# Kernel tuning notes

Measured on AMD Instinct MI355X. Metric: run time of the kernel, lower is better.

The kernel has to match this reference:

```python
import jax, jax.numpy as jnp
import numpy as np

N = 8192  # number of DAG nodes


def setup_inputs() -> dict:
    key = jax.random.key(0)
    k1, k2, k3 = jax.random.split(key, 3)
    thresholds = jax.random.normal(k1, (N,), dtype=jnp.float32)
    # children in [-1, N): -1 marks a leaf (no child)
    left = jax.random.randint(k2, (N,), -1, N, dtype=jnp.int32)
    right = jax.random.randint(k3, (N,), -1, N, dtype=jnp.int32)
    return {"thresholds": thresholds, "left": left, "right": right}


def reference(thresholds, left, right):
    # BFS fixed-point reachability from node 0, N sequential relaxation steps.
    n_nodes = left.shape[0]

    def step(reachable, _):
        # route children of reachable non-leaf nodes into a scatter; dump
        # inactive slots into the sentinel index n_nodes (dropped on slice)
        active_left = jnp.where(reachable & (left >= 0), left, n_nodes)
        active_right = jnp.where(reachable & (right >= 0), right, n_nodes)
        new_reachable = jnp.zeros(n_nodes + 1, dtype=jnp.bool_)
        new_reachable = new_reachable.at[active_left].set(True)
        new_reachable = new_reachable.at[active_right].set(True)
        new_reachable = new_reachable.at[0].set(True)
        return (new_reachable[:n_nodes] | reachable, None)

    init = jnp.zeros(n_nodes, dtype=jnp.bool_).at[0].set(True)
    mask, _ = jax.lax.scan(step, init, None, length=n_nodes)
    return mask
```

## Files before the change

kernel.cpp:

```cpp
#include <hip/hip_runtime.h>


#define NMAX   8192
#define BLK    256
#define NWORDS (NMAX / 32)
#define INNER  4

__global__ __launch_bounds__(BLK) void dag_reach_kernel(
    const int* __restrict__ left,
    const int* __restrict__ right,
    int* __restrict__ out,
    int n)
{
    __shared__ int2 sLR[NMAX];
    __shared__ unsigned int reach[NWORDS];
    __shared__ int s_changed;

    const int tid = threadIdx.x;

    for (int i = 4 * tid; i < n; i += 4 * BLK) {
        int4 l4 = *reinterpret_cast<const int4*>(left  + i);
        int4 r4 = *reinterpret_cast<const int4*>(right + i);
        sLR[i + 0] = make_int2(l4.x, r4.x);
        sLR[i + 1] = make_int2(l4.y, r4.y);
        sLR[i + 2] = make_int2(l4.z, r4.z);
        sLR[i + 3] = make_int2(l4.w, r4.w);
    }
    reach[tid] = (tid == 0) ? 1u : 0u;
    __syncthreads();

    unsigned int expanded = 0u;
    const int base = tid * 32;
    volatile unsigned int* vreach = reach;

    while (true) {
        if (tid == 0) s_changed = 0;
        __syncthreads();

        int localChanged = 0;
        #pragma unroll
        for (int it = 0; it < INNER; ++it) {
            unsigned int pend = vreach[tid] & ~expanded;
            if (pend) {
                localChanged = 1;
                expanded |= pend;
                while (pend) {
                    int b0 = __ffs(pend) - 1; pend &= pend - 1;
                    int b1 = -1, b2 = -1, b3 = -1;
                    if (pend) { b1 = __ffs(pend) - 1; pend &= pend - 1;
                        if (pend) { b2 = __ffs(pend) - 1; pend &= pend - 1;
                            if (pend) { b3 = __ffs(pend) - 1; pend &= pend - 1; } } }
                    int2 lr0 = sLR[base + b0];
                    int2 lr1 = sLR[base + (b1 < 0 ? b0 : b1)];
                    int2 lr2 = sLR[base + (b2 < 0 ? b0 : b2)];
                    int2 lr3 = sLR[base + (b3 < 0 ? b0 : b3)];
                    if (lr0.x >= 0) atomicOr(&reach[lr0.x >> 5], 1u << (lr0.x & 31));
                    if (lr0.y >= 0) atomicOr(&reach[lr0.y >> 5], 1u << (lr0.y & 31));
                    if (b1 >= 0) {
                        if (lr1.x >= 0) atomicOr(&reach[lr1.x >> 5], 1u << (lr1.x & 31));
                        if (lr1.y >= 0) atomicOr(&reach[lr1.y >> 5], 1u << (lr1.y & 31));
                    }
                    if (b2 >= 0) {
                        if (lr2.x >= 0) atomicOr(&reach[lr2.x >> 5], 1u << (lr2.x & 31));
                        if (lr2.y >= 0) atomicOr(&reach[lr2.y >> 5], 1u << (lr2.y & 31));
                    }
                    if (b3 >= 0) {
                        if (lr3.x >= 0) atomicOr(&reach[lr3.x >> 5], 1u << (lr3.x & 31));
                        if (lr3.y >= 0) atomicOr(&reach[lr3.y >> 5], 1u << (lr3.y & 31));
                    }
                }
            }
        }
        if (localChanged) s_changed = 1;
        __syncthreads();
        if (!s_changed) break;
    }

    for (int i = 4 * tid; i < n; i += 4 * BLK) {
        const unsigned w = reach[i >> 5];
        const int b = i & 31;
        *reinterpret_cast<int4*>(out + i) =
            make_int4((int)((w >> (b + 0)) & 1u),
                      (int)((w >> (b + 1)) & 1u),
                      (int)((w >> (b + 2)) & 1u),
                      (int)((w >> (b + 3)) & 1u));
    }
}

extern "C" void kernel_launch(void* const* d_in, const int* in_sizes, int n_in,
                              void* d_out, int out_size, void* d_ws, size_t ws_size,
                              hipStream_t stream)
{
    const int* left  = (const int*)d_in[1];
    const int* right = (const int*)d_in[2];
    int* out = (int*)d_out;
    const int n = in_sizes[1];

    dag_reach_kernel<<<1, BLK, 0, stream>>>(left, right, out, n);
}
```

Baseline: 74.89 us.

## Run BFS expansion in a single wavefront to drop block-wide barriers

The frontier expansion now runs on one 64-lane wavefront, with each lane owning 128 nodes (four bitmap words). Termination is decided by a wavefront vote (__any) instead of a shared flag plus two __syncthreads per round. This removes block barrier and flag overhead from the long sequential propagation chain. In exchange only 64 lanes do the work and each lane walks up to four times as many pending bits, which lowers parallelism per round.

After: 96.17 us. 1.28x slower.

```diff
diff --git a/kernel.cpp b/kernel.cpp
--- a/kernel.cpp
+++ b/kernel.cpp
@@ -4,7 +4,6 @@
 #define NMAX   8192
 #define BLK    256
 #define NWORDS (NMAX / 32)
-#define INNER  4
 
 __global__ __launch_bounds__(BLK) void dag_reach_kernel(
     const int* __restrict__ left,
@@ -14,7 +13,6 @@
 {
     __shared__ int2 sLR[NMAX];
     __shared__ unsigned int reach[NWORDS];
-    __shared__ int s_changed;
 
     const int tid = threadIdx.x;
 
@@ -26,55 +24,60 @@
         sLR[i + 2] = make_int2(l4.z, r4.z);
         sLR[i + 3] = make_int2(l4.w, r4.w);
     }
-    reach[tid] = (tid == 0) ? 1u : 0u;
+    for (int i = tid; i < NWORDS; i += BLK) reach[i] = (i == 0) ? 1u : 0u;
     __syncthreads();
 
-    unsigned int expanded = 0u;
-    const int base = tid * 32;
-    volatile unsigned int* vreach = reach;
+    if (tid < 64) {
+        const int lane  = tid;
+        const int wbase = lane * 4;
+        const int nbase = lane * 128;
+        unsigned int exp0 = 0u, exp1 = 0u, exp2 = 0u, exp3 = 0u;
+        volatile unsigned int* vreach = reach;
 
-    while (true) {
-        if (tid == 0) s_changed = 0;
-        __syncthreads();
+        while (true) {
+            unsigned int p0 = vreach[wbase + 0] & ~exp0;
+            unsigned int p1 = vreach[wbase + 1] & ~exp1;
+            unsigned int p2 = vreach[wbase + 2] & ~exp2;
+            unsigned int p3 = vreach[wbase + 3] & ~exp3;
+            unsigned long long pa = ((unsigned long long)p1 << 32) | p0;
+            unsigned long long pb = ((unsigned long long)p3 << 32) | p2;
+            if (!__any((pa | pb) != 0ull)) break;
+            exp0 |= p0; exp1 |= p1; exp2 |= p2; exp3 |= p3;
 
-        int localChanged = 0;
-        #pragma unroll
-        for (int it = 0; it < INNER; ++it) {
-            unsigned int pend = vreach[tid] & ~expanded;
-            if (pend) {
-                localChanged = 1;
-                expanded |= pend;
-                while (pend) {
-                    int b0 = __ffs(pend) - 1; pend &= pend - 1;
+            #pragma unroll
+            for (int half = 0; half < 2; ++half) {
+                unsigned long long p = half ? pb : pa;
+                const int nb = nbase + (half << 6);
+                while (p) {
+                    int b0 = __ffsll(p) - 1; p &= p - 1;
                     int b1 = -1, b2 = -1, b3 = -1;
-                    if (pend) { b1 = __ffs(pend) - 1; pend &= pend - 1;
-                        if (pend) { b2 = __ffs(pend) - 1; pend &= pend - 1;
-                            if (pend) { b3 = __ffs(pend) - 1; pend &= pend - 1; } } }
-                    int2 lr0 = sLR[base + b0];
-                    int2 lr1 = sLR[base + (b1 < 0 ? b0 : b1)];
-                    int2 lr2 = sLR[base + (b2 < 0 ? b0 : b2)];
-                    int2 lr3 = sLR[base + (b3 < 0 ? b0 : b3)];
-                    if (lr0.x >= 0) atomicOr(&reach[lr0.x >> 5], 1u << (lr0.x & 31));
-                    if (lr0.y >= 0) atomicOr(&reach[lr0.y >> 5], 1u << (lr0.y & 31));
+                    if (p) { b1 = __ffsll(p) - 1; p &= p - 1;
+                        if (p) { b2 = __ffsll(p) - 1; p &= p - 1;
+                            if (p) { b3 = __ffsll(p) - 1; p &= p - 1; } } }
+                    int2 e0 = sLR[nb + b0];
+                    int2 e1 = sLR[nb + (b1 < 0 ? b0 : b1)];
+                    int2 e2 = sLR[nb + (b2 < 0 ? b0 : b2)];
+                    int2 e3 = sLR[nb + (b3 < 0 ? b0 : b3)];
+                    if (e0.x >= 0) atomicOr(&reach[e0.x >> 5], 1u << (e0.x & 31));
+                    if (e0.y >= 0) atomicOr(&reach[e0.y >> 5], 1u << (e0.y & 31));
                     if (b1 >= 0) {
-                        if (lr1.x >= 0) atomicOr(&reach[lr1.x >> 5], 1u << (lr1.x & 31));
-                        if (lr1.y >= 0) atomicOr(&reach[lr1.y >> 5], 1u << (lr1.y & 31));
+                        if (e1.x >= 0) atomicOr(&reach[e1.x >> 5], 1u << (e1.x & 31));
+                        if (e1.y >= 0) atomicOr(&reach[e1.y >> 5], 1u << (e1.y & 31));
                     }
                     if (b2 >= 0) {
-                        if (lr2.x >= 0) atomicOr(&reach[lr2.x >> 5], 1u << (lr2.x & 31));
-                        if (lr2.y >= 0) atomicOr(&reach[lr2.y >> 5], 1u << (lr2.y & 31));
+                        if (e2.x >= 0) atomicOr(&reach[e2.x >> 5], 1u << (e2.x & 31));
+                        if (e2.y >= 0) atomicOr(&reach[e2.y >> 5], 1u << (e2.y & 31));
                     }
                     if (b3 >= 0) {
-                        if (lr3.x >= 0) atomicOr(&reach[lr3.x >> 5], 1u << (lr3.x & 31));
-                        if (lr3.y >= 0) atomicOr(&reach[lr3.y >> 5], 1u << (lr3.y & 31));
+                        if (e3.x >= 0) atomicOr(&reach[e3.x >> 5], 1u << (e3.x & 31));
+                        if (e3.y >= 0) atomicOr(&reach[e3.y >> 5], 1u << (e3.y & 31));
                     }
                 }
             }
+            __threadfence_block();
         }
-        if (localChanged) s_changed = 1;
-        __syncthreads();
-        if (!s_changed) break;
     }
+    __syncthreads();
 
     for (int i = 4 * tid; i < n; i += 4 * BLK) {
         const unsigned w = reach[i >> 5];
```

## Use 1024 threads with 8 nodes each and a triple-buffered convergence flag

Applied to the files above, without the earlier changes.

Raises the block size from 256 to 1024 threads, so each thread owns 8 nodes (a byte of a reach word) instead of 32. This shortens the per-thread serial expansion loop on the critical path. The change flag is now rotated across three shared slots and written once per wavefront via __any, which removes one __syncthreads per outer iteration. The cost is more threads contending on the shared atomics and a heavier barrier with 16 waves instead of 4.

After: 74.33 us. About the same (-0.8%).

```diff
diff --git a/kernel.cpp b/kernel.cpp
--- a/kernel.cpp
+++ b/kernel.cpp
@@ -2,7 +2,7 @@
 
 
 #define NMAX   8192
-#define BLK    256
+#define BLK    1024
 #define NWORDS (NMAX / 32)
 #define INNER  4
 
@@ -14,35 +14,49 @@
 {
     __shared__ int2 sLR[NMAX];
     __shared__ unsigned int reach[NWORDS];
-    __shared__ int s_changed;
+    __shared__ int s_flag[3];
 
     const int tid = threadIdx.x;
 
-    for (int i = 4 * tid; i < n; i += 4 * BLK) {
-        int4 l4 = *reinterpret_cast<const int4*>(left  + i);
-        int4 r4 = *reinterpret_cast<const int4*>(right + i);
-        sLR[i + 0] = make_int2(l4.x, r4.x);
-        sLR[i + 1] = make_int2(l4.y, r4.y);
-        sLR[i + 2] = make_int2(l4.z, r4.z);
-        sLR[i + 3] = make_int2(l4.w, r4.w);
+    {
+        const int i = 8 * tid;
+        if (i + 7 < n) {
+            int4 l0 = *reinterpret_cast<const int4*>(left  + i);
+            int4 l1 = *reinterpret_cast<const int4*>(left  + i + 4);
+            int4 r0 = *reinterpret_cast<const int4*>(right + i);
+            int4 r1 = *reinterpret_cast<const int4*>(right + i + 4);
+            sLR[i + 0] = make_int2(l0.x, r0.x);
+            sLR[i + 1] = make_int2(l0.y, r0.y);
+            sLR[i + 2] = make_int2(l0.z, r0.z);
+            sLR[i + 3] = make_int2(l0.w, r0.w);
+            sLR[i + 4] = make_int2(l1.x, r1.x);
+            sLR[i + 5] = make_int2(l1.y, r1.y);
+            sLR[i + 6] = make_int2(l1.z, r1.z);
+            sLR[i + 7] = make_int2(l1.w, r1.w);
+        } else {
+            for (int k = i; k < n; ++k) sLR[k] = make_int2(left[k], right[k]);
+        }
     }
-    reach[tid] = (tid == 0) ? 1u : 0u;
+    if (tid < NWORDS) reach[tid] = (tid == 0) ? 1u : 0u;
+    if (tid < 3)      s_flag[tid] = 0;
     __syncthreads();
 
+    const int word_idx = tid >> 2;
+    const int shift    = (tid & 3) * 8;
+    const int base     = tid * 8;
     unsigned int expanded = 0u;
-    const int base = tid * 32;
     volatile unsigned int* vreach = reach;
 
+    int p3 = 0;
     while (true) {
-        if (tid == 0) s_changed = 0;
-        __syncthreads();
+        const int pn3 = (p3 == 2) ? 0 : p3 + 1;
+        int ch = 0;
 
-        int localChanged = 0;
         #pragma unroll
         for (int it = 0; it < INNER; ++it) {
-            unsigned int pend = vreach[tid] & ~expanded;
+            unsigned int pend = ((vreach[word_idx] >> shift) & 0xFFu) & ~expanded;
             if (pend) {
-                localChanged = 1;
+                ch = 1;
                 expanded |= pend;
                 while (pend) {
                     int b0 = __ffs(pend) - 1; pend &= pend - 1;
@@ -50,30 +64,33 @@
                     if (pend) { b1 = __ffs(pend) - 1; pend &= pend - 1;
                         if (pend) { b2 = __ffs(pend) - 1; pend &= pend - 1;
                             if (pend) { b3 = __ffs(pend) - 1; pend &= pend - 1; } } }
-                    int2 lr0 = sLR[base + b0];
-                    int2 lr1 = sLR[base + (b1 < 0 ? b0 : b1)];
-                    int2 lr2 = sLR[base + (b2 < 0 ? b0 : b2)];
-                    int2 lr3 = sLR[base + (b3 < 0 ? b0 : b3)];
-                    if (lr0.x >= 0) atomicOr(&reach[lr0.x >> 5], 1u << (lr0.x & 31));
-                    if (lr0.y >= 0) atomicOr(&reach[lr0.y >> 5], 1u << (lr0.y & 31));
+                    int2 e0 = sLR[base + b0];
+                    int2 e1 = sLR[base + (b1 < 0 ? b0 : b1)];
+                    int2 e2 = sLR[base + (b2 < 0 ? b0 : b2)];
+                    int2 e3 = sLR[base + (b3 < 0 ? b0 : b3)];
+                    if (e0.x >= 0) atomicOr(&reach[e0.x >> 5], 1u << (e0.x & 31));
+                    if (e0.y >= 0) atomicOr(&reach[e0.y >> 5], 1u << (e0.y & 31));
                     if (b1 >= 0) {
-                        if (lr1.x >= 0) atomicOr(&reach[lr1.x >> 5], 1u << (lr1.x & 31));
-                        if (lr1.y >= 0) atomicOr(&reach[lr1.y >> 5], 1u << (lr1.y & 31));
+                        if (e1.x >= 0) atomicOr(&reach[e1.x >> 5], 1u << (e1.x & 31));
+                        if (e1.y >= 0) atomicOr(&reach[e1.y >> 5], 1u << (e1.y & 31));
                     }
                     if (b2 >= 0) {
-                        if (lr2.x >= 0) atomicOr(&reach[lr2.x >> 5], 1u << (lr2.x & 31));
-                        if (lr2.y >= 0) atomicOr(&reach[lr2.y >> 5], 1u << (lr2.y & 31));
+                        if (e2.x >= 0) atomicOr(&reach[e2.x >> 5], 1u << (e2.x & 31));
+                        if (e2.y >= 0) atomicOr(&reach[e2.y >> 5], 1u << (e2.y & 31));
                     }
                     if (b3 >= 0) {
-                        if (lr3.x >= 0) atomicOr(&reach[lr3.x >> 5], 1u << (lr3.x & 31));
-                        if (lr3.y >= 0) atomicOr(&reach[lr3.y >> 5], 1u << (lr3.y & 31));
+                        if (e3.x >= 0) atomicOr(&reach[e3.x >> 5], 1u << (e3.x & 31));
+                        if (e3.y >= 0) atomicOr(&reach[e3.y >> 5], 1u << (e3.y & 31));
                     }
                 }
             }
         }
-        if (localChanged) s_changed = 1;
+
+        if ((tid & 63) == 0) s_flag[pn3] = 0;
+        if (__any(ch) && (tid & 63) == 0) s_flag[p3] = 1;
         __syncthreads();
-        if (!s_changed) break;
+        if (!s_flag[p3]) break;
+        p3 = pn3;
     }
 
     for (int i = 4 * tid; i < n; i += 4 * BLK) {
```

## Replace barrier-synchronized BFS rounds with barrier-free counter-terminated frontier expansion

Applied to the files above, without the earlier changes.

Uses 1024 threads that each keep their 8 nodes' child indices in registers instead of staging them in shared memory. The per-round __syncthreads and changed-flag loop is replaced by an asynchronous worklist scheme. A shared outstanding-work counter is incremented before edges are pushed and decremented once each pushed edge turns out to be a duplicate or its node has been expanded, and threads spin until the counter reaches zero. This removes barrier latency and lets deep chains propagate without waiting for rounds, at the cost of continuous spinning, contended atomics on one counter, and reliance on relaxed LDS atomic visibility for correct termination.

Measured after the change: 102.6 us. 1.37x slower.

```diff
diff --git a/kernel.cpp b/kernel.cpp
--- a/kernel.cpp
+++ b/kernel.cpp
@@ -2,9 +2,8 @@
 
 
 #define NMAX   8192
-#define BLK    256
+#define BLK    1024
 #define NWORDS (NMAX / 32)
-#define INNER  4
 
 __global__ __launch_bounds__(BLK) void dag_reach_kernel(
     const int* __restrict__ left,
@@ -12,72 +11,77 @@
     int* __restrict__ out,
     int n)
 {
-    __shared__ int2 sLR[NMAX];
-    __shared__ unsigned int reach[NWORDS];
-    __shared__ int s_changed;
+    __shared__ unsigned int vis[NWORDS];
+    __shared__ int s_out;
 
-    const int tid = threadIdx.x;
+    const int tid  = threadIdx.x;
+    const int base = tid * 8;
 
-    for (int i = 4 * tid; i < n; i += 4 * BLK) {
-        int4 l4 = *reinterpret_cast<const int4*>(left  + i);
-        int4 r4 = *reinterpret_cast<const int4*>(right + i);
-        sLR[i + 0] = make_int2(l4.x, r4.x);
-        sLR[i + 1] = make_int2(l4.y, r4.y);
-        sLR[i + 2] = make_int2(l4.z, r4.z);
-        sLR[i + 3] = make_int2(l4.w, r4.w);
+    int L[8], R[8];
+    if (base + 7 < n) {
+        int4 l0 = *reinterpret_cast<const int4*>(left  + base);
+        int4 l1 = *reinterpret_cast<const int4*>(left  + base + 4);
+        int4 r0 = *reinterpret_cast<const int4*>(right + base);
+        int4 r1 = *reinterpret_cast<const int4*>(right + base + 4);
+        L[0]=l0.x; L[1]=l0.y; L[2]=l0.z; L[3]=l0.w;
+        L[4]=l1.x; L[5]=l1.y; L[6]=l1.z; L[7]=l1.w;
+        R[0]=r0.x; R[1]=r0.y; R[2]=r0.z; R[3]=r0.w;
+        R[4]=r1.x; R[5]=r1.y; R[6]=r1.z; R[7]=r1.w;
+    } else {
+        #pragma unroll
+        for (int j = 0; j < 8; ++j) {
+            L[j] = (base + j < n) ? left[base + j]  : -1;
+            R[j] = (base + j < n) ? right[base + j] : -1;
+        }
     }
-    reach[tid] = (tid == 0) ? 1u : 0u;
+
+    if (tid < NWORDS) vis[tid] = 0u;
+    if (tid == 0) { vis[0] = 1u; s_out = 1; }
     __syncthreads();
 
+    const int word  = tid >> 2;
+    const int shift = (tid & 3) * 8;
     unsigned int expanded = 0u;
-    const int base = tid * 32;
-    volatile unsigned int* vreach = reach;
 
-    while (true) {
-        if (tid == 0) s_changed = 0;
-        __syncthreads();
+    for (;;) {
+        unsigned int w = __atomic_load_n(&vis[word], __ATOMIC_RELAXED);
+        int          o = __atomic_load_n(&s_out,     __ATOMIC_RELAXED);
+        unsigned int pend = ((w >> shift) & 0xFFu) & ~expanded;
 
-        int localChanged = 0;
-        #pragma unroll
-        for (int it = 0; it < INNER; ++it) {
-            unsigned int pend = vreach[tid] & ~expanded;
-            if (pend) {
-                localChanged = 1;
-                expanded |= pend;
-                while (pend) {
-                    int b0 = __ffs(pend) - 1; pend &= pend - 1;
-                    int b1 = -1, b2 = -1, b3 = -1;
-                    if (pend) { b1 = __ffs(pend) - 1; pend &= pend - 1;
-                        if (pend) { b2 = __ffs(pend) - 1; pend &= pend - 1;
-                            if (pend) { b3 = __ffs(pend) - 1; pend &= pend - 1; } } }
-                    int2 lr0 = sLR[base + b0];
-                    int2 lr1 = sLR[base + (b1 < 0 ? b0 : b1)];
-                    int2 lr2 = sLR[base + (b2 < 0 ? b0 : b2)];
-                    int2 lr3 = sLR[base + (b3 < 0 ? b0 : b3)];
-                    if (lr0.x >= 0) atomicOr(&reach[lr0.x >> 5], 1u << (lr0.x & 31));
-                    if (lr0.y >= 0) atomicOr(&reach[lr0.y >> 5], 1u << (lr0.y & 31));
-                    if (b1 >= 0) {
-                        if (lr1.x >= 0) atomicOr(&reach[lr1.x >> 5], 1u << (lr1.x & 31));
-                        if (lr1.y >= 0) atomicOr(&reach[lr1.y >> 5], 1u << (lr1.y & 31));
-                    }
-                    if (b2 >= 0) {
-                        if (lr2.x >= 0) atomicOr(&reach[lr2.x >> 5], 1u << (lr2.x & 31));
-                        if (lr2.y >= 0) atomicOr(&reach[lr2.y >> 5], 1u << (lr2.y & 31));
-                    }
-                    if (b3 >= 0) {
-                        if (lr3.x >= 0) atomicOr(&reach[lr3.x >> 5], 1u << (lr3.x & 31));
-                        if (lr3.y >= 0) atomicOr(&reach[lr3.y >> 5], 1u << (lr3.y & 31));
-                    }
-                }
+        if (pend) {
+            expanded |= pend;
+
+            int m = 0;
+            #pragma unroll
+            for (int j = 0; j < 8; ++j) {
+                if ((pend >> j) & 1u) m += (L[j] >= 0) + (R[j] >= 0);
             }
+            if (m) atomicAdd(&s_out, m);
+
+            unsigned int oL[8], oR[8];
+            #pragma unroll
+            for (int j = 0; j < 8; ++j) {
+                const bool pj = (pend >> j) & 1u;
+                if (pj && L[j] >= 0)
+                    oL[j] = atomicOr(&vis[L[j] >> 5], 1u << (L[j] & 31));
+                if (pj && R[j] >= 0)
+                    oR[j] = atomicOr(&vis[R[j] >> 5], 1u << (R[j] & 31));
+            }
+            int d = 0;
+            #pragma unroll
+            for (int j = 0; j < 8; ++j) {
+                const bool pj = (pend >> j) & 1u;
+                if (pj && L[j] >= 0) d += (oL[j] >> (L[j] & 31)) & 1u;
+                if (pj && R[j] >= 0) d += (oR[j] >> (R[j] & 31)) & 1u;
+            }
+            atomicAdd(&s_out, -(d + __popc(pend)));
+        } else if (o == 0) {
+            break;
         }
-        if (localChanged) s_changed = 1;
-        __syncthreads();
-        if (!s_changed) break;
     }
 
     for (int i = 4 * tid; i < n; i += 4 * BLK) {
-        const unsigned w = reach[i >> 5];
+        const unsigned w = vis[i >> 5];
         const int b = i & 31;
         *reinterpret_cast<int4*>(out + i) =
             make_int4((int)((w >> (b + 0)) & 1u),
```
